# Optimization experiments

Measured on AMD Instinct MI355X. Metric: run time of the kernel, lower is better.

Reference implementation:

```python
import jax, jax.numpy as jnp
import numpy as np

B, T, D, H = 2, 2048, 1024, 16
DK = D // H


def setup_inputs() -> dict:
    key = jax.random.key(0)
    ks = jax.random.split(key, 12)
    q = jax.random.normal(ks[0], (B, T, D), jnp.float32)
    k = jax.random.normal(ks[1], (B, T, D), jnp.float32)
    v = jax.random.normal(ks[2], (B, T, D), jnp.float32)
    # padding mask [B,1,T]: 1 = valid, 0 = pad (nonzero per torch eq(0) semantics)
    lengths = jnp.array([T, (3 * T) // 4])
    mask = (jnp.arange(T)[None, None, :] < lengths[:, None, None]).astype(jnp.int32)
    s = 0.02
    Wq = jax.random.normal(ks[3], (D, D), jnp.float32) * s
    Wk = jax.random.normal(ks[4], (D, D), jnp.float32) * s
    Wv = jax.random.normal(ks[5], (D, D), jnp.float32) * s
    Wo = jax.random.normal(ks[6], (D, D), jnp.float32) * s
    bq = jnp.zeros((D,), jnp.float32)
    bk = jnp.zeros((D,), jnp.float32)
    bv = jnp.zeros((D,), jnp.float32)
    bo = jnp.zeros((D,), jnp.float32)
    return {"query": q, "key": k, "value": v, "mask": mask,
            "Wq": Wq, "bq": bq, "Wk": Wk, "bk": bk,
            "Wv": Wv, "bv": bv, "Wo": Wo, "bo": bo}


def reference(query, key, value, mask, Wq, bq, Wk, bk, Wv, bv, Wo, bo):
    # q,k,v projections -> [B, H, T, DK]
    def proj(x, W, b):
        return (x @ W.T + b).reshape(B, T, H, DK).transpose(0, 2, 1, 3)
    q = proj(query, Wq, bq)
    k = proj(key, Wk, bk)
    v = proj(value, Wv, bv)
    scores = jnp.einsum("bhqd,bhkd->bhqk", q, k) * (DK ** -0.5)  # [B,H,T,T]
    m = (mask == 0)[:, None, :, :]  # [B,1,1,T] broadcast over heads/queries
    scores = jnp.where(m, -jnp.inf, scores)
    attn = jax.nn.softmax(scores, axis=-1)
    attn = jnp.where(m, 0.0, attn)
    x = jnp.einsum("bhqk,bhkd->bhqd", attn, v)  # [B,H,T,DK]
    x = x.transpose(0, 2, 1, 3).reshape(B, T, D)
    return x @ Wo.T + bo
```

## Files before the change

### kernel.cpp

```cpp
#include <hip/hip_runtime.h>

typedef unsigned short u16;
typedef unsigned int u32;
typedef __bf16 bf16x8 __attribute__((ext_vector_type(8)));
typedef float floatx4 __attribute__((ext_vector_type(4)));

#define BB 2
#define TT 2048
#define DD 1024
#define HH 16
#define DKK 64
#define ACT (BB * TT * DD)
#define WTE (DD * DD)

__device__ inline u16 f2bf(float f) {
    union { float f; u32 u; } c; c.f = f;
    u32 r = (c.u + 0x7fffu + ((c.u >> 16) & 1u)) >> 16;
    return (u16)r;
}
__device__ inline u32 pack2bf(float a, float b) {
    return (u32)f2bf(a) | ((u32)f2bf(b) << 16);
}

typedef __attribute__((address_space(1))) const u32 gas_u32;
typedef __attribute__((address_space(3))) u32 las_u32;
__device__ __forceinline__ void gl2lds16(const u16* g, u16* l) {
    __builtin_amdgcn_global_load_lds((gas_u32*)g, (las_u32*)l, 16, 0, 0);
}

__device__ __forceinline__ u32 cvtpk_bf16(float lo, float hi) {
    u32 r;
    asm("v_cvt_pk_bf16_f32 %0, %1, %2" : "=v"(r) : "v"(lo), "v"(hi));
    return r;
}

__device__ __forceinline__ void quad_gather(u32 &a, u32 &b) {
    asm volatile("s_nop 1\n\t"
                 "v_permlane32_swap_b32 %0, %1\n\t"
                 "s_nop 1\n\t"
                 "v_permlane16_swap_b32 %0, %1"
                 : "+v"(a), "+v"(b));
}

struct CvtArgs { const float* src[7]; u16* dst[7]; };
__global__ __launch_bounds__(256) void convert_bf16(CvtArgs a) {
    int bid = blockIdx.x, t, local;
    if (bid < 768) { t = bid >> 8; local = bid & 255; }
    else { int r = bid - 768; t = 3 + (r >> 6); local = r & 63; }
    const float* s = a.src[t];
    u16* d = a.dst[t];
    const int base = local * 16384;
    for (int i = 0; i < 8; i++) {
        const int idx = base + i * 2048 + threadIdx.x * 8;
        float4 x0 = *(const float4*)(s + idx);
        float4 x1 = *(const float4*)(s + idx + 4);
        uint4 p;
        p.x = pack2bf(x0.x, x0.y); p.y = pack2bf(x0.z, x0.w);
        p.z = pack2bf(x1.x, x1.y); p.w = pack2bf(x1.z, x1.w);
        *(uint4*)(d + idx) = p;
    }
}

__global__ __launch_bounds__(256) void qkv_gemm(
    const u16* __restrict__ Qc, const u16* __restrict__ Kc,
    const u16* __restrict__ Vc,
    const u16* __restrict__ Wqc, const u16* __restrict__ Wkc,
    const u16* __restrict__ Wvc,
    const float* __restrict__ bq, const float* __restrict__ bk,
    const float* __restrict__ bv,
    u16* __restrict__ ws)
{
    __shared__ __align__(16) u16 As[128 * 32];
    __shared__ __align__(16) u16 Bs[128 * 32];
    const int z = blockIdx.z;
    const u16* A = (z == 0) ? Qc : (z == 1) ? Kc : Vc;
    const u16* W = (z == 0) ? Wqc : (z == 1) ? Wkc : Wvc;
    const float* bias = (z == 0) ? bq : (z == 1) ? bk : bv;
    u16* out = ws + (size_t)z * (size_t)BB * HH * TT * DKK;

    const int tid  = threadIdx.x;
    const int wave = tid >> 6, lane = tid & 63;
    const int quad = lane >> 4, l16 = lane & 15;
    const int wm = wave & 1, wn = wave >> 1;
    const int m0 = blockIdx.y * 128, n0 = blockIdx.x * 128;
    const int K = DD;

    const int lrow = lane >> 2, lcol = (lane & 3) * 8;
    const u16* Ag0 = A + (size_t)(m0 + wave * 16 + lrow) * K + lcol;
    const u16* Ag1 = A + (size_t)(m0 + 64 + wave * 16 + lrow) * K + lcol;
    const u16* Wg0 = W + (size_t)(n0 + wave * 16 + lrow) * K + lcol;
    const u16* Wg1 = W + (size_t)(n0 + 64 + wave * 16 + lrow) * K + lcol;
    u16* AsD0 = &As[(wave * 16) * 32];
    u16* AsD1 = &As[(64 + wave * 16) * 32];
    u16* BsD0 = &Bs[(wave * 16) * 32];
    u16* BsD1 = &Bs[(64 + wave * 16) * 32];

    floatx4 acc[4][4];
    for (int i = 0; i < 4; i++)
        for (int j = 0; j < 4; j++)
            acc[i][j] = floatx4{0.f, 0.f, 0.f, 0.f};

    for (int k0 = 0; k0 < K; k0 += 32) {
        __syncthreads();
        gl2lds16(Ag0 + k0, AsD0);
        gl2lds16(Ag1 + k0, AsD1);
        gl2lds16(Wg0 + k0, BsD0);
        gl2lds16(Wg1 + k0, BsD1);
        __syncthreads();

        bf16x8 af[4], bfr[4];
        for (int mi = 0; mi < 4; mi++)
            af[mi] = *(const bf16x8*)&As[(wm * 64 + mi * 16 + l16) * 32 + quad * 8];
        for (int ni = 0; ni < 4; ni++)
            bfr[ni] = *(const bf16x8*)&Bs[(wn * 64 + ni * 16 + l16) * 32 + quad * 8];
        for (int mi = 0; mi < 4; mi++)
            for (int ni = 0; ni < 4; ni++)
                acc[mi][ni] = __builtin_amdgcn_mfma_f32_16x16x32_bf16(
                    af[mi], bfr[ni], acc[mi][ni], 0, 0, 0);
    }

    for (int ni = 0; ni < 4; ni++) {
        const int n = n0 + wn * 64 + ni * 16 + l16;
        const float bv2 = bias[n];
        for (int mi = 0; mi < 4; mi++) {
            for (int vv = 0; vv < 4; vv++) {
                const int m = m0 + wm * 64 + mi * 16 + quad * 4 + vv;
                const float val = acc[mi][ni][vv] + bv2;
                const int b = m >> 11, t = m & 2047, h = n >> 6, dk = n & 63;
                if (z == 2)
                    out[(((size_t)(b * HH + h)) * DKK + dk) * TT + t] = f2bf(val);
                else
                    out[(((size_t)(b * HH + h)) * TT + t) * DKK + dk] = f2bf(val);
            }
        }
    }
}

__global__ __launch_bounds__(256) void out_gemm(
    const u16* __restrict__ Av, const u16* __restrict__ Wv,
    const float* __restrict__ bias, float* __restrict__ outv)
{
    __shared__ __align__(16) u16 As[128 * 32];
    __shared__ __align__(16) u16 Bs[128 * 32];
    const int tid  = threadIdx.x;
    const int wave = tid >> 6, lane = tid & 63;
    const int quad = lane >> 4, l16 = lane & 15;
    const int wm = wave & 1, wn = wave >> 1;
    const int m0 = blockIdx.y * 128, n0 = blockIdx.x * 128;
    const int K = DD, N = DD;

    const int lrow = lane >> 2, lcol = (lane & 3) * 8;
    const u16* Ag0 = Av + (size_t)(m0 + wave * 16 + lrow) * K + lcol;
    const u16* Ag1 = Av + (size_t)(m0 + 64 + wave * 16 + lrow) * K + lcol;
    const u16* Wg0 = Wv + (size_t)(n0 + wave * 16 + lrow) * K + lcol;
    const u16* Wg1 = Wv + (size_t)(n0 + 64 + wave * 16 + lrow) * K + lcol;
    u16* AsD0 = &As[(wave * 16) * 32];
    u16* AsD1 = &As[(64 + wave * 16) * 32];
    u16* BsD0 = &Bs[(wave * 16) * 32];
    u16* BsD1 = &Bs[(64 + wave * 16) * 32];

    floatx4 acc[4][4];
    for (int i = 0; i < 4; i++)
        for (int j = 0; j < 4; j++)
            acc[i][j] = floatx4{0.f, 0.f, 0.f, 0.f};

    for (int k0 = 0; k0 < K; k0 += 32) {
        __syncthreads();
        gl2lds16(Ag0 + k0, AsD0);
        gl2lds16(Ag1 + k0, AsD1);
        gl2lds16(Wg0 + k0, BsD0);
        gl2lds16(Wg1 + k0, BsD1);
        __syncthreads();

        bf16x8 af[4], bfr[4];
        for (int mi = 0; mi < 4; mi++)
            af[mi] = *(const bf16x8*)&As[(wm * 64 + mi * 16 + l16) * 32 + quad * 8];
        for (int ni = 0; ni < 4; ni++)
            bfr[ni] = *(const bf16x8*)&Bs[(wn * 64 + ni * 16 + l16) * 32 + quad * 8];
        for (int mi = 0; mi < 4; mi++)
            for (int ni = 0; ni < 4; ni++)
                acc[mi][ni] = __builtin_amdgcn_mfma_f32_16x16x32_bf16(
                    af[mi], bfr[ni], acc[mi][ni], 0, 0, 0);
    }

    for (int ni = 0; ni < 4; ni++) {
        const int n = n0 + wn * 64 + ni * 16 + l16;
        const float bv2 = bias[n];
        for (int mi = 0; mi < 4; mi++)
            for (int vv = 0; vv < 4; vv++) {
                const int m = m0 + wm * 64 + mi * 16 + quad * 4 + vv;
                outv[(size_t)m * N + n] = acc[mi][ni][vv] + bv2;
            }
    }
}

__global__ __launch_bounds__(256) void attn_kernel(
    const u16* __restrict__ Qp, const u16* __restrict__ Kp,
    const u16* __restrict__ Vpt, const int* __restrict__ mask,
    u16* __restrict__ Xa)
{
    constexpr int LDK = 72;
    __shared__ __align__(16) u16 Ks[64 * LDK];
    __shared__ __align__(16) u16 Vs[64 * LDK];
    const int tid  = threadIdx.x;
    const int wave = tid >> 6, lane = tid & 63;
    const int quad = lane >> 4, l16 = lane & 15;
    const int bid = blockIdx.x;
    const int qt = bid & 15, bh = bid >> 4;
    const int b = bh >> 4, h = bh & 15;
    const int qbase = qt * 128 + wave * 32;

    const u16* Qb = Qp + (size_t)bh * TT * DKK;
    const u16* Kb = Kp + (size_t)bh * TT * DKK;
    const u16* Vb = Vpt + (size_t)bh * DKK * TT;
    const int* mk = mask + b * TT;

    const int srow = tid >> 3, scol = (tid & 7) * 8;

    bf16x8 qf[2][2];
    #pragma unroll
    for (int mb = 0; mb < 2; mb++) {
        qf[mb][0] = *(const bf16x8*)&Qb[(size_t)(qbase + mb * 16 + l16) * DKK + quad * 8];
        qf[mb][1] = *(const bf16x8*)&Qb[(size_t)(qbase + mb * 16 + l16) * DKK + 32 + quad * 8];
    }

    floatx4 o[2][4];
    float rs[2] = {0.f, 0.f};
    for (int mb = 0; mb < 2; mb++)
        for (int i = 0; i < 4; i++)
            o[mb][i] = floatx4{0.f, 0.f, 0.f, 0.f};

    uint4 kr0 = *(const uint4*)&Kb[(size_t)srow * DKK + scol];
    uint4 kr1 = *(const uint4*)&Kb[(size_t)(32 + srow) * DKK + scol];
    uint4 vr0 = *(const uint4*)&Vb[(size_t)srow * TT + scol];
    uint4 vr1 = *(const uint4*)&Vb[(size_t)(32 + srow) * TT + scol];

    for (int ti = 0; ti < TT / 64; ti++) {
        const int k0 = ti * 64;
        __syncthreads();
        *(uint4*)&Ks[srow * LDK + scol] = kr0;
        *(uint4*)&Ks[(32 + srow) * LDK + scol] = kr1;
        *(uint4*)&Vs[srow * LDK + scol] = vr0;
        *(uint4*)&Vs[(32 + srow) * LDK + scol] = vr1;
        __syncthreads();
        if (ti + 1 < TT / 64) {
            kr0 = *(const uint4*)&Kb[(size_t)(k0 + 64 + srow) * DKK + scol];
            kr1 = *(const uint4*)&Kb[(size_t)(k0 + 96 + srow) * DKK + scol];
            vr0 = *(const uint4*)&Vb[(size_t)srow * TT + k0 + 64 + scol];
            vr1 = *(const uint4*)&Vb[(size_t)(32 + srow) * TT + k0 + 64 + scol];
        }

        const int mv0 = mk[k0 + l16];
        const int mv1 = mk[k0 + 16 + l16];
        const int mv2 = mk[k0 + 32 + l16];
        const int mv3 = mk[k0 + 48 + l16];
        if (!__any(mv0 | mv1 | mv2 | mv3)) continue;
        const bool allv = __all(mv0 && mv1 && mv2 && mv3);

        bf16x8 kf[4][2];
        #pragma unroll
        for (int c = 0; c < 4; c++) {
            kf[c][0] = *(const bf16x8*)&Ks[(c * 16 + l16) * LDK + quad * 8];
            kf[c][1] = *(const bf16x8*)&Ks[(c * 16 + l16) * LDK + 32 + quad * 8];
        }

        union { u32 w[4]; bf16x8 v; } pa[2][2];
        #pragma unroll
        for (int mb = 0; mb < 2; mb++) {
            floatx4 s[4];
            #pragma unroll
            for (int c = 0; c < 4; c++) s[c] = floatx4{0.f, 0.f, 0.f, 0.f};
            #pragma unroll
            for (int c = 0; c < 4; c++) {
                s[c] = __builtin_amdgcn_mfma_f32_16x16x32_bf16(kf[c][0], qf[mb][0], s[c], 0, 0, 0);
                s[c] = __builtin_amdgcn_mfma_f32_16x16x32_bf16(kf[c][1], qf[mb][1], s[c], 0, 0, 0);
            }

            float p[4][4];
            if (allv) {
                #pragma unroll
                for (int c = 0; c < 4; c++)
                    #pragma unroll
                    for (int v = 0; v < 4; v++)
                        p[c][v] = __expf(s[c][v] * 0.125f);
            } else {
                #pragma unroll
                for (int c = 0; c < 4; c++)
                    #pragma unroll
                    for (int v = 0; v < 4; v++)
                        p[c][v] = mk[k0 + c * 16 + quad * 4 + v]
                                      ? __expf(s[c][v] * 0.125f) : 0.f;
            }
            #pragma unroll
            for (int c = 0; c < 4; c++)
                #pragma unroll
                for (int v = 0; v < 4; v++)
                    rs[mb] += p[c][v];

            u32 A0 = cvtpk_bf16(p[0][0], p[0][1]), B0 = cvtpk_bf16(p[1][0], p[1][1]);
            u32 A1 = cvtpk_bf16(p[0][2], p[0][3]), B1 = cvtpk_bf16(p[1][2], p[1][3]);
            u32 A2 = cvtpk_bf16(p[2][0], p[2][1]), B2 = cvtpk_bf16(p[3][0], p[3][1]);
            u32 A3 = cvtpk_bf16(p[2][2], p[2][3]), B3 = cvtpk_bf16(p[3][2], p[3][3]);
            quad_gather(A0, B0);
            quad_gather(A1, B1);
            quad_gather(A2, B2);
            quad_gather(A3, B3);
            pa[mb][0].w[0] = A0; pa[mb][0].w[1] = A1; pa[mb][0].w[2] = B0; pa[mb][0].w[3] = B1;
            pa[mb][1].w[0] = A2; pa[mb][1].w[1] = A3; pa[mb][1].w[2] = B2; pa[mb][1].w[3] = B3;
        }

        #pragma unroll
        for (int nb = 0; nb < 4; nb++) {
            const bf16x8 vf0 = *(const bf16x8*)&Vs[(nb * 16 + l16) * LDK + quad * 8];
            const bf16x8 vf1 = *(const bf16x8*)&Vs[(nb * 16 + l16) * LDK + 32 + quad * 8];
            o[0][nb] = __builtin_amdgcn_mfma_f32_16x16x32_bf16(pa[0][0].v, vf0, o[0][nb], 0, 0, 0);
            o[0][nb] = __builtin_amdgcn_mfma_f32_16x16x32_bf16(pa[0][1].v, vf1, o[0][nb], 0, 0, 0);
            o[1][nb] = __builtin_amdgcn_mfma_f32_16x16x32_bf16(pa[1][0].v, vf0, o[1][nb], 0, 0, 0);
            o[1][nb] = __builtin_amdgcn_mfma_f32_16x16x32_bf16(pa[1][1].v, vf1, o[1][nb], 0, 0, 0);
        }
    }

    float inv[2][4];
    #pragma unroll
    for (int mb = 0; mb < 2; mb++) {
        rs[mb] += __shfl_xor(rs[mb], 16, 64);
        rs[mb] += __shfl_xor(rs[mb], 32, 64);
        #pragma unroll
        for (int v = 0; v < 4; v++)
            inv[mb][v] = 1.0f / __shfl(rs[mb], quad * 4 + v, 64);
    }

    #pragma unroll
    for (int mb = 0; mb < 2; mb++)
        #pragma unroll
        for (int nb = 0; nb < 4; nb++)
            #pragma unroll
            for (int v = 0; v < 4; v++) {
                const int t = qbase + mb * 16 + quad * 4 + v;
                Xa[((size_t)b * TT + t) * DD + h * DKK + nb * 16 + l16] =
                    f2bf(o[mb][nb][v] * inv[mb][v]);
            }
}

extern "C" void kernel_launch(void* const* d_in, const int* in_sizes, int n_in,
                              void* d_out, int out_size, void* d_ws, size_t ws_size,
                              hipStream_t stream) {
    const float* q    = (const float*)d_in[0];
    const float* k    = (const float*)d_in[1];
    const float* v    = (const float*)d_in[2];
    const int*   mask = (const int*)d_in[3];
    const float* Wq   = (const float*)d_in[4];
    const float* bq   = (const float*)d_in[5];
    const float* Wk   = (const float*)d_in[6];
    const float* bk   = (const float*)d_in[7];
    const float* Wv   = (const float*)d_in[8];
    const float* bv   = (const float*)d_in[9];
    const float* Wo   = (const float*)d_in[10];
    const float* bo   = (const float*)d_in[11];

    u16* Qc  = (u16*)d_ws;
    u16* Kc  = Qc + (size_t)ACT;
    u16* Vc  = Kc + (size_t)ACT;
    u16* Wqc = Vc + (size_t)ACT;
    u16* Wkc = Wqc + (size_t)WTE;
    u16* Wvc = Wkc + (size_t)WTE;
    u16* Woc = Wvc + (size_t)WTE;
    u16* Qp  = Woc + (size_t)WTE;
    u16* Kp  = Qp + (size_t)ACT;
    u16* Vpt = Kp + (size_t)ACT;
    u16* Xa  = Vpt + (size_t)ACT;

    CvtArgs ca;
    ca.src[0] = q;  ca.dst[0] = Qc;
    ca.src[1] = k;  ca.dst[1] = Kc;
    ca.src[2] = v;  ca.dst[2] = Vc;
    ca.src[3] = Wq; ca.dst[3] = Wqc;
    ca.src[4] = Wk; ca.dst[4] = Wkc;
    ca.src[5] = Wv; ca.dst[5] = Wvc;
    ca.src[6] = Wo; ca.dst[6] = Woc;
    convert_bf16<<<1024, 256, 0, stream>>>(ca);

    qkv_gemm<<<dim3(DD / 128, (BB * TT) / 128, 3), 256, 0, stream>>>(
        Qc, Kc, Vc, Wqc, Wkc, Wvc, bq, bk, bv, Qp);

    attn_kernel<<<dim3(BB * HH * (TT / 128)), 256, 0, stream>>>(Qp, Kp, Vpt, mask, Xa);

    out_gemm<<<dim3(DD / 128, (BB * TT) / 128), 256, 0, stream>>>(Xa, Woc, bo, (float*)d_out);
}
```

Before: 242.0 us.

## Double-buffer K/V tiles via direct global-to-LDS loads with XOR swizzle, 512-thread blocks

New measurement: 248.9 us. 2.9% more time.

```diff
diff --git a/kernel.cpp b/kernel.cpp
--- a/kernel.cpp
+++ b/kernel.cpp
@@ -194,28 +194,35 @@
     }
 }
 
-__global__ __launch_bounds__(256) void attn_kernel(
+__global__ __launch_bounds__(512) void attn_kernel(
     const u16* __restrict__ Qp, const u16* __restrict__ Kp,
     const u16* __restrict__ Vpt, const int* __restrict__ mask,
     u16* __restrict__ Xa)
 {
-    constexpr int LDK = 72;
-    __shared__ __align__(16) u16 Ks[64 * LDK];
-    __shared__ __align__(16) u16 Vs[64 * LDK];
+    constexpr int NT = TT / 64;
+    __shared__ __align__(16) u16 Ks[2][64 * 64];
+    __shared__ __align__(16) u16 Vs[2][64 * 64];
     const int tid  = threadIdx.x;
     const int wave = tid >> 6, lane = tid & 63;
     const int quad = lane >> 4, l16 = lane & 15;
     const int bid = blockIdx.x;
-    const int qt = bid & 15, bh = bid >> 4;
+    const int qt = bid & 7, bh = bid >> 3;
     const int b = bh >> 4, h = bh & 15;
-    const int qbase = qt * 128 + wave * 32;
+    const int qbase = qt * 256 + wave * 32;
 
     const u16* Qb = Qp + (size_t)bh * TT * DKK;
     const u16* Kb = Kp + (size_t)bh * TT * DKK;
     const u16* Vb = Vpt + (size_t)bh * DKK * TT;
     const int* mk = mask + b * TT;
 
-    const int srow = tid >> 3, scol = (tid & 7) * 8;
+    const int srow = tid >> 3, sg = tid & 7;
+    const int sgs = sg ^ (srow & 7);
+    const u16* Ksrc = Kb + (size_t)srow * DKK + sgs * 8;
+    const u16* Vsrc = Vb + (size_t)srow * TT + sgs * 8;
+
+    const int x7 = l16 & 7;
+    const int rg0 = (quad ^ x7) * 8;
+    const int rg1 = ((quad + 4) ^ x7) * 8;
 
     bf16x8 qf[2][2];
     #pragma unroll
@@ -230,38 +237,35 @@
         for (int i = 0; i < 4; i++)
             o[mb][i] = floatx4{0.f, 0.f, 0.f, 0.f};
 
-    uint4 kr0 = *(const uint4*)&Kb[(size_t)srow * DKK + scol];
-    uint4 kr1 = *(const uint4*)&Kb[(size_t)(32 + srow) * DKK + scol];
-    uint4 vr0 = *(const uint4*)&Vb[(size_t)srow * TT + scol];
-    uint4 vr1 = *(const uint4*)&Vb[(size_t)(32 + srow) * TT + scol];
-
-    for (int ti = 0; ti < TT / 64; ti++) {
+    gl2lds16(Ksrc, &Ks[0][wave * 512]);
+    gl2lds16(Vsrc, &Vs[0][wave * 512]);
+    __syncthreads();
+
+    for (int ti = 0; ti < NT; ti++) {
         const int k0 = ti * 64;
-        __syncthreads();
-        *(uint4*)&Ks[srow * LDK + scol] = kr0;
-        *(uint4*)&Ks[(32 + srow) * LDK + scol] = kr1;
-        *(uint4*)&Vs[srow * LDK + scol] = vr0;
-        *(uint4*)&Vs[(32 + srow) * LDK + scol] = vr1;
-        __syncthreads();
-        if (ti + 1 < TT / 64) {
-            kr0 = *(const uint4*)&Kb[(size_t)(k0 + 64 + srow) * DKK + scol];
-            kr1 = *(const uint4*)&Kb[(size_t)(k0 + 96 + srow) * DKK + scol];
-            vr0 = *(const uint4*)&Vb[(size_t)srow * TT + k0 + 64 + scol];
-            vr1 = *(const uint4*)&Vb[(size_t)(32 + srow) * TT + k0 + 64 + scol];
+        const int cur = ti & 1;
+
+        if (ti + 1 < NT) {
+            gl2lds16(Ksrc + (size_t)(k0 + 64) * DKK, &Ks[cur ^ 1][wave * 512]);
+            gl2lds16(Vsrc + (k0 + 64), &Vs[cur ^ 1][wave * 512]);
         }
 
         const int mv0 = mk[k0 + l16];
         const int mv1 = mk[k0 + 16 + l16];
         const int mv2 = mk[k0 + 32 + l16];
         const int mv3 = mk[k0 + 48 + l16];
-        if (!__any(mv0 | mv1 | mv2 | mv3)) continue;
+        if (!__any(mv0 | mv1 | mv2 | mv3)) {
+            __syncthreads();
+            continue;
+        }
         const bool allv = __all(mv0 && mv1 && mv2 && mv3);
 
         bf16x8 kf[4][2];
         #pragma unroll
         for (int c = 0; c < 4; c++) {
-            kf[c][0] = *(const bf16x8*)&Ks[(c * 16 + l16) * LDK + quad * 8];
-            kf[c][1] = *(const bf16x8*)&Ks[(c * 16 + l16) * LDK + 32 + quad * 8];
+            const u16* kb = &Ks[cur][(c * 16 + l16) * 64];
+            kf[c][0] = *(const bf16x8*)&kb[rg0];
+            kf[c][1] = *(const bf16x8*)&kb[rg1];
         }
 
         union { u32 w[4]; bf16x8 v; } pa[2][2];
@@ -311,13 +315,16 @@
 
         #pragma unroll
         for (int nb = 0; nb < 4; nb++) {
-            const bf16x8 vf0 = *(const bf16x8*)&Vs[(nb * 16 + l16) * LDK + quad * 8];
-            const bf16x8 vf1 = *(const bf16x8*)&Vs[(nb * 16 + l16) * LDK + 32 + quad * 8];
+            const u16* vb = &Vs[cur][(nb * 16 + l16) * 64];
+            const bf16x8 vf0 = *(const bf16x8*)&vb[rg0];
+            const bf16x8 vf1 = *(const bf16x8*)&vb[rg1];
             o[0][nb] = __builtin_amdgcn_mfma_f32_16x16x32_bf16(pa[0][0].v, vf0, o[0][nb], 0, 0, 0);
             o[0][nb] = __builtin_amdgcn_mfma_f32_16x16x32_bf16(pa[0][1].v, vf1, o[0][nb], 0, 0, 0);
             o[1][nb] = __builtin_amdgcn_mfma_f32_16x16x32_bf16(pa[1][0].v, vf0, o[1][nb], 0, 0, 0);
             o[1][nb] = __builtin_amdgcn_mfma_f32_16x16x32_bf16(pa[1][1].v, vf1, o[1][nb], 0, 0, 0);
         }
+
+        __syncthreads();
     }
 
     float inv[2][4];
@@ -383,7 +390,7 @@
     qkv_gemm<<<dim3(DD / 128, (BB * TT) / 128, 3), 256, 0, stream>>>(
         Qc, Kc, Vc, Wqc, Wkc, Wvc, bq, bk, bv, Qp);
 
-    attn_kernel<<<dim3(BB * HH * (TT / 128)), 256, 0, stream>>>(Qp, Kp, Vpt, mask, Xa);
+    attn_kernel<<<dim3(BB * HH * (TT / 256)), 512, 0, stream>>>(Qp, Kp, Vpt, mask, Xa);
 
     out_gemm<<<dim3(DD / 128, (BB * TT) / 128), 256, 0, stream>>>(Xa, Woc, bo, (float*)d_out);
 }
```
